# Kernel tuning notes

Measured on AMD Instinct MI355X. Metric: run time of the kernel, lower is better.

Reference implementation:

```python
import jax, jax.numpy as jnp
import numpy as np

B, S, D, H = 2, 2048, 1024, 16
HD = D // H  # head_dim = 64


def _rope(t, cos, sin):
    # t: (B, H, S, HD); cos/sin: (S, HD//2) -> rotate interleaved pairs
    t2 = t.reshape(*t.shape[:-1], HD // 2, 2)
    t1, t2_ = t2[..., 0], t2[..., 1]
    c = cos[None, None, :, :]
    s = sin[None, None, :, :]
    out = jnp.stack([t1 * c - t2_ * s, t1 * s + t2_ * c], axis=-1)
    return out.reshape(t.shape)


def setup_inputs() -> dict:
    key = jax.random.key(0)
    ks = jax.random.split(key, 5)
    x = jax.random.normal(ks[0], (B, S, D), dtype=jnp.float32)
    attn_mask = jnp.tril(jnp.ones((S, S), dtype=bool))  # causal
    # standard RoPE angles: pos * inv_freq
    inv_freq = 1.0 / (10000.0 ** (jnp.arange(0, HD, 2, dtype=jnp.float32) / HD))
    freqs = jnp.arange(S, dtype=jnp.float32)[:, None] * inv_freq[None, :]  # (S, HD//2)
    std = 1.0 / np.sqrt(D)
    w_qkv = jax.random.normal(ks[1], (3 * D, D), dtype=jnp.float32) * std
    b_qkv = jnp.zeros((3 * D,), dtype=jnp.float32)
    w_proj = jax.random.normal(ks[2], (D, D), dtype=jnp.float32) * std
    b_proj = jnp.zeros((D,), dtype=jnp.float32)
    return {"x": x, "attn_mask": attn_mask, "freqs": freqs,
            "w_qkv": w_qkv, "b_qkv": b_qkv, "w_proj": w_proj, "b_proj": b_proj}


def reference(x, attn_mask, freqs, w_qkv, b_qkv, w_proj, b_proj):
    # QKV projection: (B,S,D) -> (B,S,3D), split per einops pattern (three, H, HD)
    qkv = x @ w_qkv.T + b_qkv
    qkv = qkv.reshape(B, S, 3, H, HD)
    q = jnp.transpose(qkv[:, :, 0], (0, 2, 1, 3))  # (B,H,S,HD)
    k = jnp.transpose(qkv[:, :, 1], (0, 2, 1, 3))
    v = jnp.transpose(qkv[:, :, 2], (0, 2, 1, 3))
    cos, sin = jnp.cos(freqs), jnp.sin(freqs)
    q = _rope(q, cos, sin)
    k = _rope(k, cos, sin)
    scale = 1.0 / np.sqrt(HD)
    scores = jnp.einsum("bhqd,bhkd->bhqk", q, k) * scale  # (B,H,S,S)
    scores = jnp.where(attn_mask[None, None, :, :], scores, jnp.finfo(scores.dtype).min)
    attn = jax.nn.softmax(scores, axis=-1)
    out = jnp.einsum("bhqk,bhkd->bhqd", attn, v)  # (B,H,S,HD)
    out = jnp.transpose(out, (0, 2, 1, 3)).reshape(B, S, D)
    return out @ w_proj.T + b_proj
```

## Files before the change

kernel.cpp:

```cpp
#include <hip/hip_runtime.h>

#define S_LEN 2048
#define NH 16
#define HD 64
#define DMODEL 1024

typedef __bf16 bf16x8 __attribute__((ext_vector_type(8)));
typedef float floatx4 __attribute__((ext_vector_type(4)));
typedef short short8 __attribute__((ext_vector_type(8)));

__device__ inline unsigned short f2bf(float f) {
    union { float f; unsigned u; } v; v.f = f;
    unsigned u = v.u;
    unsigned r = (u + 0x7FFFu + ((u >> 16) & 1u)) >> 16;
    return (unsigned short)r;
}

__device__ __forceinline__ void gload_lds16(const void* g, void* l) {
    __builtin_amdgcn_global_load_lds(
        (const __attribute__((address_space(1))) unsigned int*)g,
        (__attribute__((address_space(3))) unsigned int*)l, 16, 0, 0);
}

#define WAITV_BAR(N) do { \
    asm volatile("s_waitcnt vmcnt(" #N ")\n\ts_barrier" ::: "memory"); \
    __builtin_amdgcn_sched_barrier(0); \
} while (0)

__device__ __forceinline__ void cvt4(const float4* __restrict__ src,
                                     uint2* __restrict__ dst, int i) {
    float4 v = src[i];
    union { unsigned short u[4]; uint2 d; } o;
    o.u[0] = f2bf(v.x); o.u[1] = f2bf(v.y); o.u[2] = f2bf(v.z); o.u[3] = f2bf(v.w);
    dst[i] = o.d;
}

__global__ __launch_bounds__(256) void prep_kernel(
    const float* __restrict__ x, const float* __restrict__ wq,
    const float* __restrict__ wp, const float* __restrict__ freqs,
    unsigned short* __restrict__ xb, unsigned short* __restrict__ wqb,
    unsigned short* __restrict__ wpb, float2* __restrict__ cs)
{
    const int tid = blockIdx.x * 256 + threadIdx.x;
    const int nth = gridDim.x * 256;
    for (int i = tid; i < (4096 * 1024) / 4; i += nth) cvt4((const float4*)x, (uint2*)xb, i);
    for (int i = tid; i < (3072 * 1024) / 4; i += nth) cvt4((const float4*)wq, (uint2*)wqb, i);
    for (int i = tid; i < (1024 * 1024) / 4; i += nth) cvt4((const float4*)wp, (uint2*)wpb, i);
    for (int i = tid; i < S_LEN * 32; i += nth) {
        const float f = freqs[i];
        float2 c; c.x = cosf(f); c.y = sinf(f);
        cs[i] = c;
    }
}

#define SROW(r) (((r) & 3) ^ (((r) >> 2) & 3))

#define QKV_STAGE(bi, kk) do { \
    unsigned short* dA_ = smem + (bi) * 8192; \
    unsigned short* dB_ = dA_ + 4096; \
    gload_lds16(ag + (kk),               dA_ + wv * 512); \
    gload_lds16(ag + 64 * DMODEL + (kk), dA_ + 2048 + wv * 512); \
    gload_lds16(bg + (kk),               dB_ + wv * 512); \
    gload_lds16(bg + 64 * DMODEL + (kk), dB_ + 2048 + wv * 512); \
} while (0)

#define QKV_COMPUTE(bi) do { \
    const unsigned short* sA_ = smem + (bi) * 8192; \
    const unsigned short* sB_ = sA_ + 4096; \
    bf16x8 af[4]; \
    _Pragma("unroll") for (int m_ = 0; m_ < 4; m_++) af[m_] = *(const bf16x8*)&sA_[aoff[m_]]; \
    _Pragma("unroll") for (int n_ = 0; n_ < 4; n_++) { \
        bf16x8 bf = *(const bf16x8*)&sB_[boff[n_]]; \
        _Pragma("unroll") for (int m_ = 0; m_ < 4; m_++) \
            acc[m_][n_] = __builtin_amdgcn_mfma_f32_16x16x32_bf16(af[m_], bf, acc[m_][n_], 0, 0, 0); \
    } \
} while (0)

__global__ __launch_bounds__(256, 3) void qkv_gemm_kernel(
    const unsigned short* __restrict__ xb, const unsigned short* __restrict__ wqb,
    const float* __restrict__ bias, const float2* __restrict__ cs,
    unsigned short* __restrict__ qb, unsigned short* __restrict__ kb,
    unsigned short* __restrict__ vb)
{
    __shared__ __align__(16) unsigned short smem[24576];

    const int t = threadIdx.x;
    const int v = (blockIdx.x & 7) * 96 + (blockIdx.x >> 3);
    const int mbase = (v / 24) * 128;
    const int nbase = (v % 24) * 128;
    const int wv = t >> 6, lane = t & 63;
    const int quad = lane >> 4, l16 = lane & 15;
    const int wr = wv >> 1, wc = wv & 1;

    floatx4 acc[4][4];
    #pragma unroll
    for (int m = 0; m < 4; m++)
        #pragma unroll
        for (int n = 0; n < 4; n++)
            #pragma unroll
            for (int r = 0; r < 4; r++) acc[m][n][r] = 0.f;

    const int srow = t >> 2;
    const int schunk = (t & 3) ^ SROW(srow);
    const unsigned short* ag = xb + (size_t)(mbase + srow) * DMODEL + schunk * 8;
    const unsigned short* bg = wqb + (size_t)(nbase + srow) * DMODEL + schunk * 8;

    const int Sl = SROW(l16);
    int aoff[4], boff[4];
    #pragma unroll
    for (int m = 0; m < 4; m++) aoff[m] = (wr * 64 + m * 16 + l16) * 32 + (quad ^ Sl) * 8;
    #pragma unroll
    for (int n = 0; n < 4; n++) boff[n] = (wc * 64 + n * 16 + l16) * 32 + (quad ^ Sl) * 8;

    QKV_STAGE(0, 0);
    QKV_STAGE(1, 32);
    for (int tb = 0; tb < 30; tb += 3) {
        WAITV_BAR(4); QKV_STAGE(2, (tb + 2) * 32); QKV_COMPUTE(0);
        WAITV_BAR(4); QKV_STAGE(0, (tb + 3) * 32); QKV_COMPUTE(1);
        WAITV_BAR(4); QKV_STAGE(1, (tb + 4) * 32); QKV_COMPUTE(2);
    }
    WAITV_BAR(4); QKV_COMPUTE(0);
    WAITV_BAR(0); QKV_COMPUTE(1);

    const int part = nbase >> 10;
    const int bidx = mbase >> 11;
    const int s0   = mbase & 2047;

    if (part == 2) {
        unsigned short* Vt = smem;
        const int hb = (nbase & 1023) >> 6;
        float bvv[4];
        #pragma unroll
        for (int nt = 0; nt < 4; nt++) bvv[nt] = bias[nbase + wc * 64 + nt * 16 + l16];
        #pragma unroll
        for (int shalf = 0; shalf < 2; shalf++) {
            __syncthreads();
            if (wr == shalf) {
                #pragma unroll
                for (int nt = 0; nt < 4; nt++) {
                    const int hdl = wc * 64 + nt * 16 + l16;
                    #pragma unroll
                    for (int m = 0; m < 4; m++)
                        #pragma unroll
                        for (int r = 0; r < 4; r++)
                            Vt[hdl * 72 + m * 16 + quad * 4 + r] = f2bf(acc[m][nt][r] + bvv[nt]);
                }
            }
            __syncthreads();
            const int hdl = t & 127, sp = t >> 7;
            const size_t bh2 = (size_t)bidx * NH + hb + (hdl >> 6);
            #pragma unroll
            for (int c = 0; c < 4; c++) {
                const int sl0 = (sp * 4 + c) * 8;
                const int sg = s0 + shalf * 64 + sl0;
                short8 vv = *(const short8*)&Vt[hdl * 72 + sl0];
                *(short8*)&vb[((bh2 * 256 + (sg >> 3)) * 64 + (hdl & 63)) * 8] = vv;
            }
        }
    } else {
        const size_t bhb = (size_t)bidx * NH;
        const int odd = l16 & 1;
        #pragma unroll
        for (int nt = 0; nt < 4; nt++) {
            const int n_ = nbase + wc * 64 + nt * 16 + l16;
            const int hd = n_ & 63;
            const size_t bh = bhb + ((n_ & 1023) >> 6);
            const float bvv = bias[n_];
            const int ci = (nt * 16 + l16) >> 1;
            #pragma unroll
            for (int m = 0; m < 4; m++) {
                #pragma unroll
                for (int r = 0; r < 4; r++) {
                    const int s = s0 + wr * 64 + m * 16 + quad * 4 + r;
                    float val = acc[m][nt][r] + bvv;
                    float other = __shfl_xor(val, 1, 64);
                    const float2 csv = cs[(size_t)s * 32 + ci];
                    float outv = odd ? fmaf(other, csv.y, val * csv.x)
                                     : fmaf(-other, csv.y, val * csv.x);
                    if (part == 0) {
                        qb[(bh * S_LEN + s) * HD + hd] = f2bf(outv * 0.125f);
                    } else {
                        kb[((bh * 8 + (hd >> 3)) * (size_t)S_LEN + s) * 8 + (hd & 7)] = f2bf(outv);
                    }
                }
            }
        }
    }
}

__global__ __launch_bounds__(256, 3) void attn_kernel(
    const unsigned short* __restrict__ qb, const unsigned short* __restrict__ kb,
    const unsigned short* __restrict__ vbk, unsigned short* __restrict__ ao)
{
    __shared__ __align__(16) unsigned short Ks[2][8 * 512];
    __shared__ __align__(16) unsigned short Vt[2][8 * 512];
    __shared__ __align__(16) unsigned short Pw[4][16 * 72];

    const int t = threadIdx.x;
    const int wv = t >> 6, lane = t & 63, quad = lane >> 4, l16 = lane & 15;
    const int qt   = 31 - (blockIdx.x >> 5);
    const int bhid = blockIdx.x & 31;
    const int h = bhid & 15, b = bhid >> 4;
    const size_t bh = (size_t)b * NH + h;
    const unsigned short* qg  = qb + bh * S_LEN * HD;
    const unsigned short* kgB = kb + bh * 8 * S_LEN * 8;
    const unsigned short* vgB = vbk + bh * 256 * 64 * 8;

    bf16x8 qf[2];
    {
        const unsigned short* q0 = qg + (size_t)(qt * 64 + wv * 16 + l16) * HD;
        qf[0] = *(const bf16x8*)&q0[quad * 8];
        qf[1] = *(const bf16x8*)&q0[32 + quad * 8];
    }

    bf16x8 ones;
    {
        union { short8 s; bf16x8 v; } o;
        for (int j = 0; j < 8; j++) o.s[j] = 0x3F80;
        ones = o.v;
    }

    floatx4 lfr = {0.f, 0.f, 0.f, 0.f};
    floatx4 Ofr[4];
    for (int nt = 0; nt < 4; nt++)
        for (int r = 0; r < 4; r++) Ofr[nt][r] = 0.f;

    const int ntiles = qt + 1;

#define ATTN_STAGE(bufi, kt_) do { \
    const int kb_ = (kt_) * 64; \
    const unsigned short* g0 = kgB + ((size_t)(2 * wv) * S_LEN + kb_ + lane) * 8; \
    gload_lds16(g0,             &Ks[bufi][(2 * wv) * 512]); \
    gload_lds16(g0 + S_LEN * 8, &Ks[bufi][(2 * wv + 1) * 512]); \
    const unsigned short* g1 = vgB + ((size_t)((kb_ >> 3) + 2 * wv) * 64 + lane) * 8; \
    gload_lds16(g1,          &Vt[bufi][(2 * wv) * 512]); \
    gload_lds16(g1 + 64 * 8, &Vt[bufi][(2 * wv + 1) * 512]); \
} while (0)

#define ATTN_COMPUTE(bufi, kt_) do { \
    const int kbase = (kt_) * 64; \
    float pex[4][4]; \
    __builtin_amdgcn_s_setprio(1); \
    _Pragma("unroll") for (int sub = 0; sub < 4; sub++) { \
        bf16x8 kf0 = *(const bf16x8*)&Ks[bufi][(0 * 4 + quad) * 512 + (sub * 16 + l16) * 8]; \
        bf16x8 kf1 = *(const bf16x8*)&Ks[bufi][(1 * 4 + quad) * 512 + (sub * 16 + l16) * 8]; \
        floatx4 sacc = {0.f, 0.f, 0.f, 0.f}; \
        sacc = __builtin_amdgcn_mfma_f32_16x16x32_bf16(kf0, qf[0], sacc, 0, 0, 0); \
        sacc = __builtin_amdgcn_mfma_f32_16x16x32_bf16(kf1, qf[1], sacc, 0, 0, 0); \
        _Pragma("unroll") for (int r = 0; r < 4; r++) pex[sub][r] = sacc[r]; \
    } \
    __builtin_amdgcn_s_setprio(0); \
    if ((kt_) == qt) { \
        const int q = qt * 64 + wv * 16 + l16; \
        _Pragma("unroll") for (int sub = 0; sub < 4; sub++) \
            _Pragma("unroll") for (int r = 0; r < 4; r++) { \
                const int key = kbase + sub * 16 + quad * 4 + r; \
                if (key > q) pex[sub][r] = -1e30f; \
            } \
    } \
    _Pragma("unroll") for (int sub = 0; sub < 4; sub++) { \
        union { unsigned short s[4]; uint2 u; } pk; \
        _Pragma("unroll") for (int r = 0; r < 4; r++) pk.s[r] = f2bf(__expf(pex[sub][r])); \
        *(uint2*)&Pw[wv][l16 * 72 + sub * 16 + quad * 4] = pk.u; \
    } \
    { \
        bf16x8 pf0 = *(const bf16x8*)&Pw[wv][l16 * 72 + quad * 8]; \
        bf16x8 pf1 = *(const bf16x8*)&Pw[wv][l16 * 72 + 32 + quad * 8]; \
        __builtin_amdgcn_s_setprio(1); \
        lfr = __builtin_amdgcn_mfma_f32_16x16x32_bf16(ones, pf0, lfr, 0, 0, 0); \
        lfr = __builtin_amdgcn_mfma_f32_16x16x32_bf16(ones, pf1, lfr, 0, 0, 0); \
        _Pragma("unroll") for (int nt = 0; nt < 4; nt++) { \
            bf16x8 v0 = *(const bf16x8*)&Vt[bufi][(0 * 4 + quad) * 512 + (nt * 16 + l16) * 8]; \
            bf16x8 v1 = *(const bf16x8*)&Vt[bufi][(1 * 4 + quad) * 512 + (nt * 16 + l16) * 8]; \
            Ofr[nt] = __builtin_amdgcn_mfma_f32_16x16x32_bf16(pf0, v0, Ofr[nt], 0, 0, 0); \
            Ofr[nt] = __builtin_amdgcn_mfma_f32_16x16x32_bf16(pf1, v1, Ofr[nt], 0, 0, 0); \
        } \
        __builtin_amdgcn_s_setprio(0); \
    } \
} while (0)

    ATTN_STAGE(0, 0);
    __syncthreads();
    for (int kt = 0; kt < ntiles; ) {
        if (kt + 1 < ntiles) ATTN_STAGE(1, kt + 1);
        ATTN_COMPUTE(0, kt);
        kt++;
        if (kt >= ntiles) break;
        __syncthreads();
        if (kt + 1 < ntiles) ATTN_STAGE(0, kt + 1);
        ATTN_COMPUTE(1, kt);
        kt++;
        if (kt >= ntiles) break;
        __syncthreads();
    }

    float linv[4];
    #pragma unroll
    for (int r = 0; r < 4; r++) {
        float lq = __shfl(lfr[0], (lane & 48) | (quad * 4 + r), 64);
        linv[r] = 1.f / lq;
    }
    #pragma unroll
    for (int nt = 0; nt < 4; nt++)
        #pragma unroll
        for (int r = 0; r < 4; r++) {
            const int s = qt * 64 + wv * 16 + quad * 4 + r;
            ao[((size_t)b * S_LEN + s) * DMODEL + h * HD + nt * 16 + l16] =
                f2bf(Ofr[nt][r] * linv[r]);
        }
#undef ATTN_STAGE
#undef ATTN_COMPUTE
}

#define PROJ_STAGE(bi, kk) do { \
    unsigned short* dA_ = smem + (bi) * 6144; \
    unsigned short* dB_ = dA_ + 4096; \
    gload_lds16(ag + (kk),               dA_ + wv * 512); \
    gload_lds16(ag + 64 * DMODEL + (kk), dA_ + 2048 + wv * 512); \
    gload_lds16(bg + (kk),               dB_ + wv * 512); \
} while (0)

#define PROJ_COMPUTE(bi) do { \
    const unsigned short* sA_ = smem + (bi) * 6144; \
    const unsigned short* sB_ = sA_ + 4096; \
    bf16x8 af[4]; \
    _Pragma("unroll") for (int m_ = 0; m_ < 4; m_++) af[m_] = *(const bf16x8*)&sA_[aoff[m_]]; \
    _Pragma("unroll") for (int n_ = 0; n_ < 2; n_++) { \
        bf16x8 bf = *(const bf16x8*)&sB_[boff[n_]]; \
        _Pragma("unroll") for (int m_ = 0; m_ < 4; m_++) \
            acc[m_][n_] = __builtin_amdgcn_mfma_f32_16x16x32_bf16(af[m_], bf, acc[m_][n_], 0, 0, 0); \
    } \
} while (0)

__global__ __launch_bounds__(256, 3) void proj_kernel(
    const unsigned short* __restrict__ a, const unsigned short* __restrict__ wpb,
    const float* __restrict__ bias, float* __restrict__ out)
{
    __shared__ __align__(16) unsigned short smem[18432];

    const int t = threadIdx.x;
    const int v = (blockIdx.x & 7) * 64 + (blockIdx.x >> 3);
    const int mbase = (v >> 4) * 128;
    const int nbase = (v & 15) * 64;
    const int wv = t >> 6, lane = t & 63, quad = lane >> 4, l16 = lane & 15;
    const int wr = wv >> 1, wc = wv & 1;

    floatx4 acc[4][2];
    #pragma unroll
    for (int m = 0; m < 4; m++)
        #pragma unroll
        for (int n = 0; n < 2; n++)
            #pragma unroll
            for (int r = 0; r < 4; r++) acc[m][n][r] = 0.f;

    const int srow = t >> 2;
    const int schunk = (t & 3) ^ SROW(srow);
    const unsigned short* ag = a + (size_t)(mbase + srow) * DMODEL + schunk * 8;
    const unsigned short* bg = wpb + (size_t)(nbase + srow) * DMODEL + schunk * 8;

    const int Sl = SROW(l16);
    int aoff[4], boff[2];
    #pragma unroll
    for (int m = 0; m < 4; m++) aoff[m] = (wr * 64 + m * 16 + l16) * 32 + (quad ^ Sl) * 8;
    #pragma unroll
    for (int n = 0; n < 2; n++) boff[n] = (wc * 32 + n * 16 + l16) * 32 + (quad ^ Sl) * 8;

    PROJ_STAGE(0, 0);
    PROJ_STAGE(1, 32);
    for (int tb = 0; tb < 30; tb += 3) {
        WAITV_BAR(3); PROJ_STAGE(2, (tb + 2) * 32); PROJ_COMPUTE(0);
        WAITV_BAR(3); PROJ_STAGE(0, (tb + 3) * 32); PROJ_COMPUTE(1);
        WAITV_BAR(3); PROJ_STAGE(1, (tb + 4) * 32); PROJ_COMPUTE(2);
    }
    WAITV_BAR(3); PROJ_COMPUTE(0);
    WAITV_BAR(0); PROJ_COMPUTE(1);

    #pragma unroll
    for (int n = 0; n < 2; n++) {
        const int nn = nbase + wc * 32 + n * 16 + l16;
        const float bvv = bias[nn];
        #pragma unroll
        for (int m = 0; m < 4; m++)
            #pragma unroll
            for (int r = 0; r < 4; r++)
                out[(size_t)(mbase + wr * 64 + m * 16 + quad * 4 + r) * DMODEL + nn] =
                    acc[m][n][r] + bvv;
    }
}

extern "C" void kernel_launch(void* const* d_in, const int* in_sizes, int n_in,
                              void* d_out, int out_size, void* d_ws, size_t ws_size,
                              hipStream_t stream) {
    const float* x      = (const float*)d_in[0];
    const float* freqs  = (const float*)d_in[2];
    const float* w_qkv  = (const float*)d_in[3];
    const float* b_qkv  = (const float*)d_in[4];
    const float* w_proj = (const float*)d_in[5];
    const float* b_proj = (const float*)d_in[6];
    float* out = (float*)d_out;

    unsigned short* ws = (unsigned short*)d_ws;
    const size_t HSZ = (size_t)2 * NH * S_LEN * HD;
    unsigned short* qb  = ws;
    unsigned short* kb  = ws + HSZ;
    unsigned short* vb  = ws + 2 * HSZ;
    unsigned short* ao  = ws + 3 * HSZ;
    unsigned short* xb  = ws + 4 * HSZ;
    unsigned short* wqb = xb + (size_t)4096 * 1024;
    unsigned short* wpb = wqb + (size_t)3072 * 1024;
    float2* cs = (float2*)(wpb + (size_t)1024 * 1024);

    prep_kernel<<<2048, 256, 0, stream>>>(x, w_qkv, w_proj, freqs, xb, wqb, wpb, cs);
    qkv_gemm_kernel<<<768, 256, 0, stream>>>(xb, wqb, b_qkv, cs, qb, kb, vb);
    attn_kernel<<<1024, 256, 0, stream>>>(qb, kb, vb, ao);
    proj_kernel<<<512, 256, 0, stream>>>(ao, wpb, b_proj, out);
}
```

Baseline: 196.7 us.

## Enlarge QKV GEMM tiles to 256x256 with 512-thread blocks and double buffering

```diff
diff --git a/kernel.cpp b/kernel.cpp
--- a/kernel.cpp
+++ b/kernel.cpp
@@ -56,105 +56,113 @@
 #define SROW(r) (((r) & 3) ^ (((r) >> 2) & 3))
 
 #define QKV_STAGE(bi, kk) do { \
-    unsigned short* dA_ = smem + (bi) * 8192; \
-    unsigned short* dB_ = dA_ + 4096; \
-    gload_lds16(ag + (kk),               dA_ + wv * 512); \
-    gload_lds16(ag + 64 * DMODEL + (kk), dA_ + 2048 + wv * 512); \
-    gload_lds16(bg + (kk),               dB_ + wv * 512); \
-    gload_lds16(bg + 64 * DMODEL + (kk), dB_ + 2048 + wv * 512); \
+    unsigned short* A_ = smem + (bi) * 16384; \
+    unsigned short* B_ = A_ + 8192; \
+    gload_lds16(agp0 + (kk), A_ + wv * 512); \
+    gload_lds16(agp1 + (kk), A_ + 4096 + wv * 512); \
+    gload_lds16(bgp0 + (kk), B_ + wv * 512); \
+    gload_lds16(bgp1 + (kk), B_ + 4096 + wv * 512); \
 } while (0)
 
 #define QKV_COMPUTE(bi) do { \
-    const unsigned short* sA_ = smem + (bi) * 8192; \
-    const unsigned short* sB_ = sA_ + 4096; \
-    bf16x8 af[4]; \
-    _Pragma("unroll") for (int m_ = 0; m_ < 4; m_++) af[m_] = *(const bf16x8*)&sA_[aoff[m_]]; \
-    _Pragma("unroll") for (int n_ = 0; n_ < 4; n_++) { \
-        bf16x8 bf = *(const bf16x8*)&sB_[boff[n_]]; \
-        _Pragma("unroll") for (int m_ = 0; m_ < 4; m_++) \
-            acc[m_][n_] = __builtin_amdgcn_mfma_f32_16x16x32_bf16(af[m_], bf, acc[m_][n_], 0, 0, 0); \
-    } \
-} while (0)
-
-__global__ __launch_bounds__(256, 3) void qkv_gemm_kernel(
+    const unsigned short* A_ = smem + (bi) * 16384; \
+    const unsigned short* B_ = A_ + 8192; \
+    bf16x8 af[8], bf[4]; \
+    _Pragma("unroll") for (int m_ = 0; m_ < 8; m_++) af[m_] = *(const bf16x8*)&A_[aoff[m_]]; \
+    _Pragma("unroll") for (int n_ = 0; n_ < 4; n_++) bf[n_] = *(const bf16x8*)&B_[boff[n_]]; \
+    __builtin_amdgcn_s_setprio(1); \
+    _Pragma("unroll") for (int n_ = 0; n_ < 4; n_++) \
+        _Pragma("unroll") for (int m_ = 0; m_ < 8; m_++) \
+            acc[m_][n_] = __builtin_amdgcn_mfma_f32_16x16x32_bf16(af[m_], bf[n_], acc[m_][n_], 0, 0, 0); \
+    __builtin_amdgcn_s_setprio(0); \
+} while (0)
+
+__global__ __launch_bounds__(512, 2) void qkv_gemm_kernel(
     const unsigned short* __restrict__ xb, const unsigned short* __restrict__ wqb,
     const float* __restrict__ bias, const float2* __restrict__ cs,
     unsigned short* __restrict__ qb, unsigned short* __restrict__ kb,
     unsigned short* __restrict__ vb)
 {
-    __shared__ __align__(16) unsigned short smem[24576];
+    __shared__ __align__(16) unsigned short smem[32768];
 
     const int t = threadIdx.x;
-    const int v = (blockIdx.x & 7) * 96 + (blockIdx.x >> 3);
-    const int mbase = (v / 24) * 128;
-    const int nbase = (v % 24) * 128;
+    const int v = (blockIdx.x & 7) * 24 + (blockIdx.x >> 3);
+    const int mbase = (v / 12) * 256;
+    const int nbase = (v % 12) * 256;
     const int wv = t >> 6, lane = t & 63;
     const int quad = lane >> 4, l16 = lane & 15;
-    const int wr = wv >> 1, wc = wv & 1;
-
-    floatx4 acc[4][4];
-    #pragma unroll
-    for (int m = 0; m < 4; m++)
+    const int wr = wv >> 2, wcc = wv & 3;
+
+    floatx4 acc[8][4];
+    #pragma unroll
+    for (int m = 0; m < 8; m++)
         #pragma unroll
         for (int n = 0; n < 4; n++)
             #pragma unroll
             for (int r = 0; r < 4; r++) acc[m][n][r] = 0.f;
 
-    const int srow = t >> 2;
-    const int schunk = (t & 3) ^ SROW(srow);
-    const unsigned short* ag = xb + (size_t)(mbase + srow) * DMODEL + schunk * 8;
-    const unsigned short* bg = wqb + (size_t)(nbase + srow) * DMODEL + schunk * 8;
-
-    const int Sl = SROW(l16);
-    int aoff[4], boff[4];
-    #pragma unroll
-    for (int m = 0; m < 4; m++) aoff[m] = (wr * 64 + m * 16 + l16) * 32 + (quad ^ Sl) * 8;
-    #pragma unroll
-    for (int n = 0; n < 4; n++) boff[n] = (wc * 64 + n * 16 + l16) * 32 + (quad ^ Sl) * 8;
+    const int r0 = t >> 2;
+    const int sc0 = (t & 3) ^ ((r0 >> 1) & 3);
+    const unsigned short* agp0 = xb + (size_t)(mbase + r0) * DMODEL + sc0 * 8;
+    const unsigned short* agp1 = xb + (size_t)(mbase + r0 + 128) * DMODEL + sc0 * 8;
+    const unsigned short* bgp0 = wqb + (size_t)(nbase + r0) * DMODEL + sc0 * 8;
+    const unsigned short* bgp1 = wqb + (size_t)(nbase + r0 + 128) * DMODEL + sc0 * 8;
+
+    int aoff[8], boff[4];
+    #pragma unroll
+    for (int m = 0; m < 8; m++) {
+        const int row = wr * 128 + m * 16 + l16;
+        aoff[m] = row * 32 + ((quad ^ ((row >> 1) & 3)) * 8);
+    }
+    #pragma unroll
+    for (int n = 0; n < 4; n++) {
+        const int row = wcc * 64 + n * 16 + l16;
+        boff[n] = row * 32 + ((quad ^ ((row >> 1) & 3)) * 8);
+    }
 
     QKV_STAGE(0, 0);
-    QKV_STAGE(1, 32);
-    for (int tb = 0; tb < 30; tb += 3) {
-        WAITV_BAR(4); QKV_STAGE(2, (tb + 2) * 32); QKV_COMPUTE(0);
-        WAITV_BAR(4); QKV_STAGE(0, (tb + 3) * 32); QKV_COMPUTE(1);
-        WAITV_BAR(4); QKV_STAGE(1, (tb + 4) * 32); QKV_COMPUTE(2);
-    }
-    WAITV_BAR(4); QKV_COMPUTE(0);
-    WAITV_BAR(0); QKV_COMPUTE(1);
+    __syncthreads();
+    for (int kt = 0; kt < 32; kt++) {
+        if (kt + 1 < 32) QKV_STAGE((kt + 1) & 1, (kt + 1) * 32);
+        QKV_COMPUTE(kt & 1);
+        __syncthreads();
+    }
 
     const int part = nbase >> 10;
     const int bidx = mbase >> 11;
     const int s0   = mbase & 2047;
+    const int hb   = (nbase & 1023) >> 6;
 
     if (part == 2) {
         unsigned short* Vt = smem;
-        const int hb = (nbase & 1023) >> 6;
         float bvv[4];
         #pragma unroll
-        for (int nt = 0; nt < 4; nt++) bvv[nt] = bias[nbase + wc * 64 + nt * 16 + l16];
-        #pragma unroll
-        for (int shalf = 0; shalf < 2; shalf++) {
+        for (int nt = 0; nt < 4; nt++) bvv[nt] = bias[nbase + wcc * 64 + nt * 16 + l16];
+        #pragma unroll
+        for (int ch = 0; ch < 4; ch++) {
             __syncthreads();
-            if (wr == shalf) {
+            if (wr == (ch >> 1)) {
+                const int mb = (ch & 1) * 4;
                 #pragma unroll
                 for (int nt = 0; nt < 4; nt++) {
-                    const int hdl = wc * 64 + nt * 16 + l16;
+                    const int hdl = wcc * 64 + nt * 16 + l16;
                     #pragma unroll
-                    for (int m = 0; m < 4; m++)
+                    for (int mm = 0; mm < 4; mm++)
                         #pragma unroll
                         for (int r = 0; r < 4; r++)
-                            Vt[hdl * 72 + m * 16 + quad * 4 + r] = f2bf(acc[m][nt][r] + bvv[nt]);
+                            Vt[hdl * 72 + mm * 16 + quad * 4 + r] =
+                                f2bf(acc[mb + mm][nt][r] + bvv[nt]);
                 }
             }
             __syncthreads();
-            const int hdl = t & 127, sp = t >> 7;
-            const size_t bh2 = (size_t)bidx * NH + hb + (hdl >> 6);
+            const int hd = t & 255, sp = t >> 8;
+            const size_t bh2 = (size_t)bidx * NH + hb + (hd >> 6);
             #pragma unroll
             for (int c = 0; c < 4; c++) {
                 const int sl0 = (sp * 4 + c) * 8;
-                const int sg = s0 + shalf * 64 + sl0;
-                short8 vv = *(const short8*)&Vt[hdl * 72 + sl0];
-                *(short8*)&vb[((bh2 * 256 + (sg >> 3)) * 64 + (hdl & 63)) * 8] = vv;
+                const int sg = s0 + ch * 64 + sl0;
+                short8 vv = *(const short8*)&Vt[hd * 72 + sl0];
+                *(short8*)&vb[((bh2 * 256 + (sg >> 3)) * 64 + (hd & 63)) * 8] = vv;
             }
         }
     } else {
@@ -162,16 +170,16 @@
         const int odd = l16 & 1;
         #pragma unroll
         for (int nt = 0; nt < 4; nt++) {
-            const int n_ = nbase + wc * 64 + nt * 16 + l16;
+            const int n_ = nbase + wcc * 64 + nt * 16 + l16;
             const int hd = n_ & 63;
             const size_t bh = bhb + ((n_ & 1023) >> 6);
             const float bvv = bias[n_];
-            const int ci = (nt * 16 + l16) >> 1;
+            const int ci = hd >> 1;
             #pragma unroll
-            for (int m = 0; m < 4; m++) {
+            for (int m = 0; m < 8; m++) {
                 #pragma unroll
                 for (int r = 0; r < 4; r++) {
-                    const int s = s0 + wr * 64 + m * 16 + quad * 4 + r;
+                    const int s = s0 + wr * 128 + m * 16 + quad * 4 + r;
                     float val = acc[m][nt][r] + bvv;
                     float other = __shfl_xor(val, 1, 64);
                     const float2 csv = cs[(size_t)s * 32 + ci];
@@ -411,7 +419,7 @@
     float2* cs = (float2*)(wpb + (size_t)1024 * 1024);
 
     prep_kernel<<<2048, 256, 0, stream>>>(x, w_qkv, w_proj, freqs, xb, wqb, wpb, cs);
-    qkv_gemm_kernel<<<768, 256, 0, stream>>>(xb, wqb, b_qkv, cs, qb, kb, vb);
+    qkv_gemm_kernel<<<192, 512, 0, stream>>>(xb, wqb, b_qkv, cs, qb, kb, vb);
     attn_kernel<<<1024, 256, 0, stream>>>(qb, kb, vb, ao);
     proj_kernel<<<512, 256, 0, stream>>>(ao, wpb, b_proj, out);
 }
```

New measurement: 219.2 us. +11.5%, slower.

## Double attention query tile to 128 rows per block for K/V reuse

Applied to the files above, without the earlier changes.

```diff
diff --git a/kernel.cpp b/kernel.cpp
--- a/kernel.cpp
+++ b/kernel.cpp
@@ -194,11 +194,12 @@
 {
     __shared__ __align__(16) unsigned short Ks[2][8 * 512];
     __shared__ __align__(16) unsigned short Vt[2][8 * 512];
-    __shared__ __align__(16) unsigned short Pw[4][16 * 72];
+    __shared__ __align__(16) unsigned short Pw[4][32 * 72];
 
     const int t = threadIdx.x;
     const int wv = t >> 6, lane = t & 63, quad = lane >> 4, l16 = lane & 15;
-    const int qt   = 31 - (blockIdx.x >> 5);
+    const int qp = 15 - (blockIdx.x >> 5);
+    const int qbase = qp * 128;
     const int bhid = blockIdx.x & 31;
     const int h = bhid & 15, b = bhid >> 4;
     const size_t bh = (size_t)b * NH + h;
@@ -206,11 +207,12 @@
     const unsigned short* kgB = kb + bh * 8 * S_LEN * 8;
     const unsigned short* vgB = vbk + bh * 256 * 64 * 8;
 
-    bf16x8 qf[2];
-    {
-        const unsigned short* q0 = qg + (size_t)(qt * 64 + wv * 16 + l16) * HD;
-        qf[0] = *(const bf16x8*)&q0[quad * 8];
-        qf[1] = *(const bf16x8*)&q0[32 + quad * 8];
+    bf16x8 qf[2][2];
+    #pragma unroll
+    for (int cg = 0; cg < 2; cg++) {
+        const unsigned short* q0 = qg + (size_t)(qbase + wv * 32 + cg * 16 + l16) * HD;
+        qf[cg][0] = *(const bf16x8*)&q0[quad * 8];
+        qf[cg][1] = *(const bf16x8*)&q0[32 + quad * 8];
     }
 
     bf16x8 ones;
@@ -220,12 +222,16 @@
         ones = o.v;
     }
 
-    floatx4 lfr = {0.f, 0.f, 0.f, 0.f};
-    floatx4 Ofr[4];
-    for (int nt = 0; nt < 4; nt++)
-        for (int r = 0; r < 4; r++) Ofr[nt][r] = 0.f;
-
-    const int ntiles = qt + 1;
+    floatx4 lfr[2];
+    floatx4 Ofr[2][4];
+    #pragma unroll
+    for (int cg = 0; cg < 2; cg++) {
+        for (int r = 0; r < 4; r++) lfr[cg][r] = 0.f;
+        for (int nt = 0; nt < 4; nt++)
+            for (int r = 0; r < 4; r++) Ofr[cg][nt][r] = 0.f;
+    }
+
+    const int ntiles = (qbase >> 6) + 2;
 
 #define ATTN_STAGE(bufi, kt_) do { \
     const int kb_ = (kt_) * 64; \
@@ -239,41 +245,50 @@
 
 #define ATTN_COMPUTE(bufi, kt_) do { \
     const int kbase = (kt_) * 64; \
-    float pex[4][4]; \
+    float pex[2][4][4]; \
     __builtin_amdgcn_s_setprio(1); \
     _Pragma("unroll") for (int sub = 0; sub < 4; sub++) { \
         bf16x8 kf0 = *(const bf16x8*)&Ks[bufi][(0 * 4 + quad) * 512 + (sub * 16 + l16) * 8]; \
         bf16x8 kf1 = *(const bf16x8*)&Ks[bufi][(1 * 4 + quad) * 512 + (sub * 16 + l16) * 8]; \
-        floatx4 sacc = {0.f, 0.f, 0.f, 0.f}; \
-        sacc = __builtin_amdgcn_mfma_f32_16x16x32_bf16(kf0, qf[0], sacc, 0, 0, 0); \
-        sacc = __builtin_amdgcn_mfma_f32_16x16x32_bf16(kf1, qf[1], sacc, 0, 0, 0); \
-        _Pragma("unroll") for (int r = 0; r < 4; r++) pex[sub][r] = sacc[r]; \
+        _Pragma("unroll") for (int cg = 0; cg < 2; cg++) { \
+            floatx4 sacc = {0.f, 0.f, 0.f, 0.f}; \
+            sacc = __builtin_amdgcn_mfma_f32_16x16x32_bf16(kf0, qf[cg][0], sacc, 0, 0, 0); \
+            sacc = __builtin_amdgcn_mfma_f32_16x16x32_bf16(kf1, qf[cg][1], sacc, 0, 0, 0); \
+            _Pragma("unroll") for (int r = 0; r < 4; r++) pex[cg][sub][r] = sacc[r]; \
+        } \
     } \
     __builtin_amdgcn_s_setprio(0); \
-    if ((kt_) == qt) { \
-        const int q = qt * 64 + wv * 16 + l16; \
-        _Pragma("unroll") for (int sub = 0; sub < 4; sub++) \
-            _Pragma("unroll") for (int r = 0; r < 4; r++) { \
-                const int key = kbase + sub * 16 + quad * 4 + r; \
-                if (key > q) pex[sub][r] = -1e30f; \
-            } \
-    } \
-    _Pragma("unroll") for (int sub = 0; sub < 4; sub++) { \
-        union { unsigned short s[4]; uint2 u; } pk; \
-        _Pragma("unroll") for (int r = 0; r < 4; r++) pk.s[r] = f2bf(__expf(pex[sub][r])); \
-        *(uint2*)&Pw[wv][l16 * 72 + sub * 16 + quad * 4] = pk.u; \
+    _Pragma("unroll") for (int cg = 0; cg < 2; cg++) { \
+        if (kbase + 63 > qbase + wv * 32 + cg * 16) {    \
+            const int q = qbase + wv * 32 + cg * 16 + l16; \
+            _Pragma("unroll") for (int sub = 0; sub < 4; sub++) \
+                _Pragma("unroll") for (int r = 0; r < 4; r++) { \
+                    const int key = kbase + sub * 16 + quad * 4 + r; \
+                    if (key > q) pex[cg][sub][r] = -1e30f; \
+                } \
+        } \
+        _Pragma("unroll") for (int sub = 0; sub < 4; sub++) { \
+            union { unsigned short s[4]; uint2 u; } pk; \
+            _Pragma("unroll") for (int r = 0; r < 4; r++) pk.s[r] = f2bf(__expf(pex[cg][sub][r])); \
+            *(uint2*)&Pw[wv][(cg * 16 + l16) * 72 + sub * 16 + quad * 4] = pk.u; \
+        } \
     } \
     { \
-        bf16x8 pf0 = *(const bf16x8*)&Pw[wv][l16 * 72 + quad * 8]; \
-        bf16x8 pf1 = *(const bf16x8*)&Pw[wv][l16 * 72 + 32 + quad * 8]; \
+        bf16x8 pf[2][2]; \
+        _Pragma("unroll") for (int cg = 0; cg < 2; cg++) { \
+            pf[cg][0] = *(const bf16x8*)&Pw[wv][(cg * 16 + l16) * 72 + quad * 8]; \
+            pf[cg][1] = *(const bf16x8*)&Pw[wv][(cg * 16 + l16) * 72 + 32 + quad * 8]; \
+            lfr[cg] = __builtin_amdgcn_mfma_f32_16x16x32_bf16(ones, pf[cg][0], lfr[cg], 0, 0, 0); \
+            lfr[cg] = __builtin_amdgcn_mfma_f32_16x16x32_bf16(ones, pf[cg][1], lfr[cg], 0, 0, 0); \
+        } \
         __builtin_amdgcn_s_setprio(1); \
-        lfr = __builtin_amdgcn_mfma_f32_16x16x32_bf16(ones, pf0, lfr, 0, 0, 0); \
-        lfr = __builtin_amdgcn_mfma_f32_16x16x32_bf16(ones, pf1, lfr, 0, 0, 0); \
         _Pragma("unroll") for (int nt = 0; nt < 4; nt++) { \
             bf16x8 v0 = *(const bf16x8*)&Vt[bufi][(0 * 4 + quad) * 512 + (nt * 16 + l16) * 8]; \
             bf16x8 v1 = *(const bf16x8*)&Vt[bufi][(1 * 4 + quad) * 512 + (nt * 16 + l16) * 8]; \
-            Ofr[nt] = __builtin_amdgcn_mfma_f32_16x16x32_bf16(pf0, v0, Ofr[nt], 0, 0, 0); \
-            Ofr[nt] = __builtin_amdgcn_mfma_f32_16x16x32_bf16(pf1, v1, Ofr[nt], 0, 0, 0); \
+            _Pragma("unroll") for (int cg = 0; cg < 2; cg++) { \
+                Ofr[cg][nt] = __builtin_amdgcn_mfma_f32_16x16x32_bf16(pf[cg][0], v0, Ofr[cg][nt], 0, 0, 0); \
+                Ofr[cg][nt] = __builtin_amdgcn_mfma_f32_16x16x32_bf16(pf[cg][1], v1, Ofr[cg][nt], 0, 0, 0); \
+            } \
         } \
         __builtin_amdgcn_s_setprio(0); \
     } \
@@ -294,20 +309,24 @@
         __syncthreads();
     }
 
-    float linv[4];
-    #pragma unroll
-    for (int r = 0; r < 4; r++) {
-        float lq = __shfl(lfr[0], (lane & 48) | (quad * 4 + r), 64);
-        linv[r] = 1.f / lq;
-    }
-    #pragma unroll
-    for (int nt = 0; nt < 4; nt++)
+    float linv[2][4];
+    #pragma unroll
+    for (int cg = 0; cg < 2; cg++)
         #pragma unroll
         for (int r = 0; r < 4; r++) {
-            const int s = qt * 64 + wv * 16 + quad * 4 + r;
-            ao[((size_t)b * S_LEN + s) * DMODEL + h * HD + nt * 16 + l16] =
-                f2bf(Ofr[nt][r] * linv[r]);
+            float lq = __shfl(lfr[cg][0], (lane & 48) | (quad * 4 + r), 64);
+            linv[cg][r] = 1.f / lq;
         }
+    #pragma unroll
+    for (int cg = 0; cg < 2; cg++)
+        #pragma unroll
+        for (int nt = 0; nt < 4; nt++)
+            #pragma unroll
+            for (int r = 0; r < 4; r++) {
+                const int s = qbase + wv * 32 + cg * 16 + quad * 4 + r;
+                ao[((size_t)b * S_LEN + s) * DMODEL + h * HD + nt * 16 + l16] =
+                    f2bf(Ofr[cg][nt][r] * linv[cg][r]);
+            }
 #undef ATTN_STAGE
 #undef ATTN_COMPUTE
 }
@@ -412,6 +431,6 @@
 
     prep_kernel<<<2048, 256, 0, stream>>>(x, w_qkv, w_proj, freqs, xb, wqb, wpb, cs);
     qkv_gemm_kernel<<<768, 256, 0, stream>>>(xb, wqb, b_qkv, cs, qb, kb, vb);
-    attn_kernel<<<1024, 256, 0, stream>>>(qb, kb, vb, ao);
+    attn_kernel<<<512, 256, 0, stream>>>(qb, kb, vb, ao);
     proj_kernel<<<512, 256, 0, stream>>>(ao, wpb, b_proj, out);
 }
```

Result: slower. 202.9 us (+3.2%).
